# Kernel optimization log

Measured on AMD Instinct MI355X. Metric: run time of the kernel, lower is better.

The kernel has to match this reference:

```python
import jax, jax.numpy as jnp
import numpy as np

CAP_FACTOR = 1.25


def _moe_top1(x, wg, w1, b1, w2, b2):
    """Top-1 switch MoE with capacity-based token dropping.
    x: [T, d]; wg: [d, E]; w1: [E, d, f]; b1: [E, f]; w2: [E, f, d]; b2: [E, d].
    """
    T, d = x.shape
    E = wg.shape[1]
    cap = int(CAP_FACTOR * T / E)
    probs = jax.nn.softmax(x @ wg, axis=-1)            # [T, E]
    idx = jnp.argmax(probs, axis=-1)                   # [T] expert assignment
    gate = jnp.max(probs, axis=-1)                     # [T] gate prob
    oh = jax.nn.one_hot(idx, E, dtype=jnp.int32)       # [T, E]
    # position of each token within its expert's buffer
    pos = (jnp.cumsum(oh, axis=0) * oh).sum(-1) - 1    # [T]
    keep = pos < cap                                   # drop tokens over capacity
    pos_w = jnp.where(keep, pos, cap)                  # dropped -> overflow slot
    # dispatch: scatter tokens into per-expert buffers [E, cap+1, d]
    buf = jnp.zeros((E, cap + 1, d), dtype=x.dtype).at[idx, pos_w].set(x)
    buf = buf[:, :cap]                                 # slice off overflow slot
    # grouped expert FFN
    h = jax.nn.relu(jnp.einsum('ecd,edf->ecf', buf, w1) + b1[:, None, :])
    eo = jnp.einsum('ecf,efd->ecd', h, w2) + b2[:, None, :]
    # combine: gather each token's expert output, scale by gate prob, zero dropped
    pos_g = jnp.minimum(pos_w, cap - 1)
    out = eo[idx, pos_g] * (gate * keep.astype(x.dtype))[:, None]
    return out


def setup_inputs():
    key = jax.random.key(0)
    ks = jax.random.split(key, 12)
    B, S, d, dff, E1, E2 = 8, 2048, 1024, 4096, 8, 16
    s = lambda fan: np.float32(1.0 / np.sqrt(fan))
    return dict(
        x=jax.random.normal(ks[0], (B, S, d), jnp.float32),
        y=jax.random.randint(ks[1], (B,), 0, d),
        wg1=jax.random.normal(ks[2], (d, E1), jnp.float32) * s(d),
        w1a=jax.random.normal(ks[3], (E1, d, dff), jnp.float32) * s(d),
        b1a=jnp.zeros((E1, dff), jnp.float32),
        w2a=jax.random.normal(ks[4], (E1, dff, d), jnp.float32) * s(dff),
        b2a=jnp.zeros((E1, d), jnp.float32),
        wg2=jax.random.normal(ks[5], (d, E2), jnp.float32) * s(d),
        w1b=jax.random.normal(ks[6], (E2, d, dff), jnp.float32) * s(d),
        b1b=jnp.zeros((E2, dff), jnp.float32),
        w2b=jax.random.normal(ks[7], (E2, dff, d), jnp.float32) * s(dff),
        b2b=jnp.zeros((E2, d), jnp.float32),
    )


def reference(x, y, wg1, w1a, b1a, w2a, b2a, wg2, w1b, b1b, w2b, b2b):
    B, S, d = x.shape
    xf = x.reshape(B * S, d)
    m1 = _moe_top1(xf, wg1, w1a, b1a, w2a, b2a)        # moe1(x)
    m2 = _moe_top1(m1, wg2, w1b, b1b, w2b, b2b)        # moe2(moe_out)
    resid = x + m2.reshape(B, S, d)                    # residual add
    sent = resid.mean(axis=1)                          # [B, d] mean-pool -> logits
    logp = jax.nn.log_softmax(sent, axis=-1)
    return -logp[jnp.arange(B), y].mean()              # cross-entropy loss
```

## Files before the change

kernel.cpp:

```cpp
#include <hip/hip_runtime.h>
#include <hip/hip_bf16.h>
#include <cstdint>
#include <cstddef>

#define B_    8
#define S_    2048
#define D_    1024
#define DFF_  4096
#define E1_   8
#define E2_   16
#define T_    (B_*S_)
#define CAP1_ 2560
#define CAP2_ 1280
#define EC_   20480

typedef __bf16 bf16x8 __attribute__((ext_vector_type(8)));
typedef float  f32x4  __attribute__((ext_vector_type(4)));

__device__ __forceinline__ unsigned short f2bf(float x) {
  return __builtin_bit_cast(unsigned short, (__bf16)x);
}

template<int E>
__global__ __launch_bounds__(256)
void gate_kernel(const float* __restrict__ X, const float* __restrict__ WG,
                 int* __restrict__ idxO, float* __restrict__ gateO) {
  const int lane = threadIdx.x & 63;
  const int wv   = threadIdx.x >> 6;
  const int t    = blockIdx.x * 4 + wv;
  const float* xr = X + (size_t)t * D_;
  float acc[E];
#pragma unroll
  for (int e = 0; e < E; ++e) acc[e] = 0.f;
#pragma unroll
  for (int i = 0; i < 4; ++i) {
    float4 xv = *(const float4*)(xr + i * 256 + lane * 4);
    int kb = i * 256 + lane * 4;
#pragma unroll
    for (int j = 0; j < 4; ++j) {
      float xs = (&xv.x)[j];
      const float* wr = WG + (size_t)(kb + j) * E;
#pragma unroll
      for (int e = 0; e < E; ++e) acc[e] += xs * wr[e];
    }
  }
#pragma unroll
  for (int e = 0; e < E; ++e) {
    float v = acc[e];
#pragma unroll
    for (int s = 32; s >= 1; s >>= 1) v += __shfl_xor(v, s, 64);
    acc[e] = v;
  }
  if (lane == 0) {
    float mx = acc[0]; int mi = 0;
#pragma unroll
    for (int e = 1; e < E; ++e) if (acc[e] > mx) { mx = acc[e]; mi = e; }
    float s = 0.f;
#pragma unroll
    for (int e = 0; e < E; ++e) s += expf(acc[e] - mx);
    idxO[t]  = mi;
    gateO[t] = 1.0f / s;
  }
}

__global__ __launch_bounds__(1024)
void scan_kernel(const int* __restrict__ idx, int E, int cap,
                 int* __restrict__ pos, int* __restrict__ kept) {
  __shared__ int cnt[16][17];
  __shared__ int gbase[16];
  const int tid = threadIdx.x;
  const int w = tid >> 6, lane = tid & 63;
  if (tid < E) gbase[tid] = 0;
  __syncthreads();
  const unsigned long long lt = (lane == 63) ? 0xFFFFFFFFFFFFFFFFull >> 1
                                             : ((1ull << lane) - 1ull);
  for (int it = 0; it < T_ / 1024; ++it) {
    int t = it * 1024 + tid;
    int mi = idx[t];
    int rank = 0;
    for (int e = 0; e < E; ++e) {
      unsigned long long m = __ballot(mi == e);
      if (lane == 0) cnt[w][e] = __popcll(m);
      if (mi == e) rank = __popcll(m & lt);
    }
    __syncthreads();
    int off = 0;
    for (int w2 = 0; w2 < w; ++w2) off += cnt[w2][mi];
    pos[t] = gbase[mi] + off + rank;
    __syncthreads();
    if (tid < E) {
      int tot = 0;
      for (int w2 = 0; w2 < 16; ++w2) tot += cnt[w2][tid];
      gbase[tid] += tot;
    }
    __syncthreads();
  }
  if (tid < E) kept[tid] = min(gbase[tid], cap);
}

__global__ __launch_bounds__(64)
void scatter_kernel(const float* __restrict__ X, const int* __restrict__ idx,
                    const int* __restrict__ pos, int cap,
                    unsigned short* __restrict__ xbuf, int* __restrict__ tokmap,
                    float* __restrict__ mzero) {
  const int t = blockIdx.x;
  const int lane = threadIdx.x;
  const int p = pos[t];
  if (p < cap) {
    const size_t dst = ((size_t)idx[t] * cap + p) * D_;
    const float* xr = X + (size_t)t * D_;
#pragma unroll
    for (int i = 0; i < 4; ++i) {
      float4 v = *(const float4*)(xr + i * 256 + lane * 4);
      ushort4 o;
      o.x = f2bf(v.x); o.y = f2bf(v.y); o.z = f2bf(v.z); o.w = f2bf(v.w);
      *(ushort4*)(xbuf + dst + i * 256 + lane * 4) = o;
    }
    if (lane == 0) tokmap[(size_t)idx[t] * cap + p] = t;
  } else {
    float4 z = {0.f, 0.f, 0.f, 0.f};
    float* mr = mzero + (size_t)t * D_;
#pragma unroll
    for (int i = 0; i < 4; ++i) *(float4*)(mr + i * 256 + lane * 4) = z;
  }
}

__global__ __launch_bounds__(256)
void wtrans_kernel(const float* __restrict__ src, unsigned short* __restrict__ dst,
                   int K, int N) {
  __shared__ float t[64][65];
  const int tid = threadIdx.x;
  const size_t eo = (size_t)blockIdx.z * K * N;
  const int k0 = blockIdx.y * 64, n0 = blockIdx.x * 64;
  const float* s = src + eo + (size_t)k0 * N + n0;
  unsigned short* d = dst + eo + (size_t)n0 * K + k0;
#pragma unroll
  for (int i = 0; i < 4; ++i) {
    int k = i * 16 + (tid >> 4);
    int n4 = (tid & 15) * 4;
    float4 v = *(const float4*)(s + (size_t)k * N + n4);
    t[k][n4] = v.x; t[k][n4 + 1] = v.y; t[k][n4 + 2] = v.z; t[k][n4 + 3] = v.w;
  }
  __syncthreads();
#pragma unroll
  for (int i = 0; i < 4; ++i) {
    int n = i * 16 + (tid >> 4);
    int k4 = (tid & 15) * 4;
    ushort4 o;
    o.x = f2bf(t[k4][n]);     o.y = f2bf(t[k4 + 1][n]);
    o.z = f2bf(t[k4 + 2][n]); o.w = f2bf(t[k4 + 3][n]);
    *(ushort4*)(d + (size_t)n * K + k4) = o;
  }
}

template<int MODE>
__global__ __launch_bounds__(256)
void moe_gemm(const unsigned short* __restrict__ A,
              const unsigned short* __restrict__ BT,
              const float* __restrict__ bias, int K, int N, int cap, int nbcnt,
              const int* __restrict__ kept,
              unsigned short* __restrict__ Hout, float* __restrict__ Mout,
              const int* __restrict__ tokmap, const float* __restrict__ gate) {
  __shared__ char smem[16384];
  char* As = smem;
  char* Bs = smem + 8192;
  const int tid  = threadIdx.x;
  const int lane = tid & 63;
  const int wv   = tid >> 6;
  const int wr   = wv >> 1, wc = wv & 1;

  const int nwg = gridDim.x;
  const int wg  = (blockIdx.x & 7) * (nwg >> 3) + (blockIdx.x >> 3);
  const int per_grp = nbcnt * 4;
  const int grp = wg / per_grp;
  const int rem = wg - grp * per_grp;
  const int mb  = grp * 4 + (rem & 3);
  const int nb  = rem >> 2;

  const int e  = (mb * 128) / cap;
  const int r0 = mb * 128 - e * cap;
  const int kept_e = kept[e];
  if (r0 >= kept_e) return;
  const unsigned short* Ab = A + (size_t)(mb * 128) * K;
  const unsigned short* Bb = BT + ((size_t)e * N + (size_t)nb * 128) * K;

  f32x4 acc[4][4];
#pragma unroll
  for (int m = 0; m < 4; ++m)
#pragma unroll
    for (int n = 0; n < 4; ++n) acc[m][n] = (f32x4){0.f, 0.f, 0.f, 0.f};

  const int srow = tid >> 2;
  const int scb  = (tid & 3) * 16;

  for (int k0 = 0; k0 < K; k0 += 32) {
#pragma unroll
    for (int p = 0; p < 2; ++p) {
      const int row = p * 64 + srow;
      const int sw  = scb ^ ((row & 3) << 4);
      const unsigned short* ga = Ab + (size_t)row * K + k0 + (sw >> 1);
      const unsigned short* gb = Bb + (size_t)row * K + k0 + (sw >> 1);
      char* la = As + (size_t)(p * 256 + (tid & ~63)) * 16;
      char* lb = Bs + (size_t)(p * 256 + (tid & ~63)) * 16;
      __builtin_amdgcn_global_load_lds((const __attribute__((address_space(1))) void*)ga,
                                       (__attribute__((address_space(3))) void*)la,
                                       16, 0, 0);
      __builtin_amdgcn_global_load_lds((const __attribute__((address_space(1))) void*)gb,
                                       (__attribute__((address_space(3))) void*)lb,
                                       16, 0, 0);
    }
    __syncthreads();

    bf16x8 af[4], bfr[4];
    const int g16 = (lane >> 4) * 16;
    const int r16 = lane & 15;
#pragma unroll
    for (int m = 0; m < 4; ++m) {
      const int row = wr * 64 + m * 16 + r16;
      af[m] = *(const bf16x8*)(As + row * 64 + (g16 ^ ((row & 3) << 4)));
      const int col = wc * 64 + m * 16 + r16;
      bfr[m] = *(const bf16x8*)(Bs + col * 64 + (g16 ^ ((col & 3) << 4)));
    }
#pragma unroll
    for (int m = 0; m < 4; ++m)
#pragma unroll
      for (int n = 0; n < 4; ++n)
        acc[m][n] = __builtin_amdgcn_mfma_f32_16x16x32_bf16(af[m], bfr[n], acc[m][n], 0, 0, 0);
    __syncthreads();
  }

  const int r16 = lane & 15, rg = lane >> 4;
  float bv[4];
#pragma unroll
  for (int n = 0; n < 4; ++n)
    bv[n] = bias[(size_t)e * N + nb * 128 + wc * 64 + n * 16 + r16];

#pragma unroll
  for (int m = 0; m < 4; ++m) {
#pragma unroll
    for (int r = 0; r < 4; ++r) {
      const int lrow = wr * 64 + m * 16 + rg * 4 + r;
      if (MODE == 0) {
        unsigned short* orow = Hout + (size_t)(mb * 128 + lrow) * N + nb * 128;
#pragma unroll
        for (int n = 0; n < 4; ++n) {
          float v = acc[m][n][r] + bv[n];
          orow[wc * 64 + n * 16 + r16] = f2bf(fmaxf(v, 0.f));
        }
      } else {
        const int lr = r0 + lrow;
        if (lr < kept_e) {
          const int tok = tokmap[mb * 128 + lrow];
          const float gsc = gate[tok];
          float* orow = Mout + (size_t)tok * N + nb * 128;
#pragma unroll
          for (int n = 0; n < 4; ++n)
            orow[wc * 64 + n * 16 + r16] = (acc[m][n][r] + bv[n]) * gsc;
        }
      }
    }
  }
}

__global__ __launch_bounds__(256)
void reduce_kernel(const float* __restrict__ X, const float* __restrict__ M2,
                   float* __restrict__ sent) {
  const int c = blockIdx.x * 256 + threadIdx.x;
  const int b = blockIdx.z;
  const int s0 = blockIdx.y * 128;
  float a = 0.f;
  size_t base = ((size_t)b * S_ + s0) * D_ + c;
  for (int s = 0; s < 128; ++s) a += X[base + (size_t)s * D_] + M2[base + (size_t)s * D_];
  atomicAdd(&sent[b * D_ + c], a * (1.0f / (float)S_));
}

__global__ __launch_bounds__(64)
void loss_kernel(const float* __restrict__ sent, const int* __restrict__ y,
                 float* __restrict__ out) {
  const int lane = threadIdx.x;
  float total = 0.f;
  for (int b = 0; b < B_; ++b) {
    const float* s = sent + b * D_;
    float v[16];
    float mx = -1e30f;
#pragma unroll
    for (int i = 0; i < 16; ++i) { v[i] = s[lane + i * 64]; mx = fmaxf(mx, v[i]); }
#pragma unroll
    for (int sh = 32; sh >= 1; sh >>= 1) mx = fmaxf(mx, __shfl_xor(mx, sh, 64));
    float sm = 0.f;
#pragma unroll
    for (int i = 0; i < 16; ++i) sm += expf(v[i] - mx);
#pragma unroll
    for (int sh = 32; sh >= 1; sh >>= 1) sm += __shfl_xor(sm, sh, 64);
    total += logf(sm) + mx - s[y[b]];
  }
  if (lane == 0) out[0] = total * (1.0f / (float)B_);
}

extern "C" void kernel_launch(void* const* d_in, const int* in_sizes, int n_in,
                              void* d_out, int out_size, void* d_ws, size_t ws_size,
                              hipStream_t stream) {
  const float* x   = (const float*)d_in[0];
  const int*   y   = (const int*)d_in[1];
  const float* wg1 = (const float*)d_in[2];
  const float* w1a = (const float*)d_in[3];
  const float* b1a = (const float*)d_in[4];
  const float* w2a = (const float*)d_in[5];
  const float* b2a = (const float*)d_in[6];
  const float* wg2 = (const float*)d_in[7];
  const float* w1b = (const float*)d_in[8];
  const float* b1b = (const float*)d_in[9];
  const float* w2b = (const float*)d_in[10];
  const float* b2b = (const float*)d_in[11];
  float* out = (float*)d_out;
  (void)in_sizes; (void)n_in; (void)out_size; (void)ws_size;

  char* base = (char*)d_ws;
  size_t o = 0;
  auto alloc = [&](size_t bytes) { size_t r = o; o = (o + bytes + 255) & ~(size_t)255; return r; };
  int*   idx1    = (int*)  (base + alloc((size_t)T_ * 4));
  int*   pos1    = (int*)  (base + alloc((size_t)T_ * 4));
  float* gate1   = (float*)(base + alloc((size_t)T_ * 4));
  int*   idx2    = (int*)  (base + alloc((size_t)T_ * 4));
  int*   pos2    = (int*)  (base + alloc((size_t)T_ * 4));
  float* gate2   = (float*)(base + alloc((size_t)T_ * 4));
  int*   kept1   = (int*)  (base + alloc(64 * 4));
  int*   kept2   = (int*)  (base + alloc(64 * 4));
  int*   tokmap1 = (int*)  (base + alloc((size_t)EC_ * 4));
  int*   tokmap2 = (int*)  (base + alloc((size_t)EC_ * 4));
  float* sent    = (float*)(base + alloc((size_t)B_ * D_ * 4));
  float* m1      = (float*)(base + alloc((size_t)T_ * D_ * 4));
  unsigned short* xbuf = (unsigned short*)(base + alloc((size_t)EC_ * D_ * 2));
  unsigned short* h    = (unsigned short*)(base + alloc((size_t)EC_ * DFF_ * 2));
  unsigned short* wT   = (unsigned short*)(base + alloc((size_t)E2_ * D_ * DFF_ * 2));

  hipMemsetAsync(sent, 0, (size_t)B_ * D_ * 4, stream);

  gate_kernel<E1_><<<T_ / 4, 256, 0, stream>>>(x, wg1, idx1, gate1);
  scan_kernel<<<1, 1024, 0, stream>>>(idx1, E1_, CAP1_, pos1, kept1);
  scatter_kernel<<<T_, 64, 0, stream>>>(x, idx1, pos1, CAP1_, xbuf, tokmap1, m1);
  wtrans_kernel<<<dim3(DFF_ / 64, D_ / 64, E1_), 256, 0, stream>>>(w1a, wT, D_, DFF_);
  moe_gemm<0><<<(DFF_ / 128) * (EC_ / 128), 256, 0, stream>>>(
      xbuf, wT, b1a, D_, DFF_, CAP1_, DFF_ / 128, kept1, h, nullptr, nullptr, nullptr);
  wtrans_kernel<<<dim3(D_ / 64, DFF_ / 64, E1_), 256, 0, stream>>>(w2a, wT, DFF_, D_);
  moe_gemm<1><<<(D_ / 128) * (EC_ / 128), 256, 0, stream>>>(
      h, wT, b2a, DFF_, D_, CAP1_, D_ / 128, kept1, nullptr, m1, tokmap1, gate1);

  gate_kernel<E2_><<<T_ / 4, 256, 0, stream>>>(m1, wg2, idx2, gate2);
  scan_kernel<<<1, 1024, 0, stream>>>(idx2, E2_, CAP2_, pos2, kept2);
  scatter_kernel<<<T_, 64, 0, stream>>>(m1, idx2, pos2, CAP2_, xbuf, tokmap2, m1);
  wtrans_kernel<<<dim3(DFF_ / 64, D_ / 64, E2_), 256, 0, stream>>>(w1b, wT, D_, DFF_);
  moe_gemm<0><<<(DFF_ / 128) * (EC_ / 128), 256, 0, stream>>>(
      xbuf, wT, b1b, D_, DFF_, CAP2_, DFF_ / 128, kept2, h, nullptr, nullptr, nullptr);
  wtrans_kernel<<<dim3(D_ / 64, DFF_ / 64, E2_), 256, 0, stream>>>(w2b, wT, DFF_, D_);
  moe_gemm<1><<<(D_ / 128) * (EC_ / 128), 256, 0, stream>>>(
      h, wT, b2b, DFF_, D_, CAP2_, D_ / 128, kept2, nullptr, m1, tokmap2, gate2);

  reduce_kernel<<<dim3(D_ / 256, S_ / 128, B_), 256, 0, stream>>>(x, m1, sent);
  loss_kernel<<<1, 64, 0, stream>>>(sent, y, out);
}
```

Measured before the change: 1.542 ms.

## Double-buffer LDS staging with BK=64 and MFMA priority in MoE GEMM

Result: faster. 1.381 ms (-10.4%).

```diff
diff --git a/kernel.cpp b/kernel.cpp
--- a/kernel.cpp
+++ b/kernel.cpp
@@ -154,16 +154,14 @@
 }
 
 template<int MODE>
-__global__ __launch_bounds__(256)
+__global__ __launch_bounds__(256, 2)
 void moe_gemm(const unsigned short* __restrict__ A,
               const unsigned short* __restrict__ BT,
               const float* __restrict__ bias, int K, int N, int cap, int nbcnt,
               const int* __restrict__ kept,
               unsigned short* __restrict__ Hout, float* __restrict__ Mout,
               const int* __restrict__ tokmap, const float* __restrict__ gate) {
-  __shared__ char smem[16384];
-  char* As = smem;
-  char* Bs = smem + 8192;
+  __shared__ char smem[65536];
   const int tid  = threadIdx.x;
   const int lane = tid & 63;
   const int wv   = tid >> 6;
@@ -190,18 +188,17 @@
 #pragma unroll
     for (int n = 0; n < 4; ++n) acc[m][n] = (f32x4){0.f, 0.f, 0.f, 0.f};
 
-  const int srow = tid >> 2;
-  const int scb  = (tid & 3) * 16;
-
-  for (int k0 = 0; k0 < K; k0 += 32) {
-#pragma unroll
-    for (int p = 0; p < 2; ++p) {
-      const int row = p * 64 + srow;
-      const int sw  = scb ^ ((row & 3) << 4);
-      const unsigned short* ga = Ab + (size_t)row * K + k0 + (sw >> 1);
-      const unsigned short* gb = Bb + (size_t)row * K + k0 + (sw >> 1);
-      char* la = As + (size_t)(p * 256 + (tid & ~63)) * 16;
-      char* lb = Bs + (size_t)(p * 256 + (tid & ~63)) * 16;
+  auto stage = [&](int buf, int k0) {
+#pragma unroll
+    for (int j = 0; j < 4; ++j) {
+      const int c   = j * 256 + tid;
+      const int row = c >> 3;
+      const int cc  = c & 7;
+      const int scol = (cc ^ (row & 7)) << 3;
+      const unsigned short* ga = Ab + (size_t)row * K + k0 + scol;
+      const unsigned short* gb = Bb + (size_t)row * K + k0 + scol;
+      char* la = smem + buf * 32768 + (j * 256 + (tid & ~63)) * 16;
+      char* lb = la + 16384;
       __builtin_amdgcn_global_load_lds((const __attribute__((address_space(1))) void*)ga,
                                        (__attribute__((address_space(3))) void*)la,
                                        16, 0, 0);
@@ -209,27 +206,52 @@
                                        (__attribute__((address_space(3))) void*)lb,
                                        16, 0, 0);
     }
-    __syncthreads();
-
-    bf16x8 af[4], bfr[4];
-    const int g16 = (lane >> 4) * 16;
-    const int r16 = lane & 15;
+  };
+
+  const int NT = K >> 6;
+  stage(0, 0);
+  __syncthreads();
+  int cur = 0;
+
+  const int g16 = (lane >> 4) * 16;
+  const int r16 = lane & 15;
+
+  for (int t = 0; t < NT; ++t) {
+    if (t + 1 < NT) stage(cur ^ 1, (t + 1) << 6);
+
+    const char* As = smem + cur * 32768;
+    const char* Bs = As + 16384;
+    bf16x8 af[4][2], bfr[4][2];
 #pragma unroll
     for (int m = 0; m < 4; ++m) {
       const int row = wr * 64 + m * 16 + r16;
-      af[m] = *(const bf16x8*)(As + row * 64 + (g16 ^ ((row & 3) << 4)));
-      const int col = wc * 64 + m * 16 + r16;
-      bfr[m] = *(const bf16x8*)(Bs + col * 64 + (g16 ^ ((col & 3) << 4)));
-    }
-#pragma unroll
-    for (int m = 0; m < 4; ++m)
-#pragma unroll
-      for (int n = 0; n < 4; ++n)
-        acc[m][n] = __builtin_amdgcn_mfma_f32_16x16x32_bf16(af[m], bfr[n], acc[m][n], 0, 0, 0);
+      const int sw  = (row & 7) << 4;
+#pragma unroll
+      for (int ks = 0; ks < 2; ++ks)
+        af[m][ks] = *(const bf16x8*)(As + row * 128 + ((ks * 64 + g16) ^ sw));
+    }
+#pragma unroll
+    for (int n = 0; n < 4; ++n) {
+      const int row = wc * 64 + n * 16 + r16;
+      const int sw  = (row & 7) << 4;
+#pragma unroll
+      for (int ks = 0; ks < 2; ++ks)
+        bfr[n][ks] = *(const bf16x8*)(Bs + row * 128 + ((ks * 64 + g16) ^ sw));
+    }
+    __builtin_amdgcn_s_setprio(1);
+#pragma unroll
+    for (int ks = 0; ks < 2; ++ks)
+#pragma unroll
+      for (int m = 0; m < 4; ++m)
+#pragma unroll
+        for (int n = 0; n < 4; ++n)
+          acc[m][n] = __builtin_amdgcn_mfma_f32_16x16x32_bf16(af[m][ks], bfr[n][ks], acc[m][n], 0, 0, 0);
+    __builtin_amdgcn_s_setprio(0);
     __syncthreads();
-  }
-
-  const int r16 = lane & 15, rg = lane >> 4;
+    cur ^= 1;
+  }
+
+  const int rg = lane >> 4;
   float bv[4];
 #pragma unroll
   for (int n = 0; n < 4; ++n)
```

## Rewrite MoE GEMM with 256x256 tiles and a double-buffered LDS pipeline

Applied to the files above, without the earlier changes.

Measured after the change: 1.293 ms. -16.2%, faster.

```diff
diff --git a/kernel.cpp b/kernel.cpp
--- a/kernel.cpp
+++ b/kernel.cpp
@@ -153,21 +153,56 @@
   }
 }
 
+#define STG(BASEPTR, H, KT, SLOT) do {                                          \
+    const unsigned short* _s = (BASEPTR) + (size_t)((H) * 128) * K + (KT) + st_off; \
+    __builtin_amdgcn_global_load_lds((const __attribute__((address_space(1))) void*)_s, \
+        (__attribute__((address_space(3))) void*)(smem + (SLOT) + dst0), 16, 0, 0);   \
+    __builtin_amdgcn_global_load_lds((const __attribute__((address_space(1))) void*)(_s + (size_t)64 * K), \
+        (__attribute__((address_space(3))) void*)(smem + (SLOT) + 8192 + dst0), 16, 0, 0); \
+  } while (0)
+
+#define RDA(BUF, MH) do { _Pragma("unroll")                                     \
+    for (int m_ = 0; m_ < 4; ++m_) {                                            \
+      const char* _p = smem + (BUF) * 65536 + aslot + ((MH) * 4 + m_) * 2048;   \
+      af[m_][0] = *(const bf16x8*)(_p + va);                                    \
+      af[m_][1] = *(const bf16x8*)(_p + (va ^ 64)); } } while (0)
+
+#define RDB(BUF, NH) do { _Pragma("unroll")                                     \
+    for (int j_ = 0; j_ < 2; ++j_) {                                            \
+      const char* _p = smem + (BUF) * 65536 + bslot + ((NH) * 2 + j_) * 2048;   \
+      bf[(NH) * 2 + j_][0] = *(const bf16x8*)(_p + vb);                         \
+      bf[(NH) * 2 + j_][1] = *(const bf16x8*)(_p + (vb ^ 64)); } } while (0)
+
+#define QUAD(MH, NH) do {                                                       \
+    __builtin_amdgcn_s_setprio(1);                                              \
+    _Pragma("unroll") for (int m_ = 0; m_ < 4; ++m_)                            \
+    _Pragma("unroll") for (int j_ = 0; j_ < 2; ++j_)                            \
+    _Pragma("unroll") for (int k_ = 0; k_ < 2; ++k_)                            \
+      acc[(MH) * 4 + m_][(NH) * 2 + j_] = __builtin_amdgcn_mfma_f32_16x16x32_bf16( \
+          af[m_][k_], bf[(NH) * 2 + j_][k_], acc[(MH) * 4 + m_][(NH) * 2 + j_], 0, 0, 0); \
+    __builtin_amdgcn_s_setprio(0);                                              \
+  } while (0)
+
+#define LGKM0 do { asm volatile("s_waitcnt lgkmcnt(0)" ::: "memory");           \
+                   __builtin_amdgcn_sched_barrier(0); } while (0)
+#define BAR   __builtin_amdgcn_s_barrier()
+#define VM4   asm volatile("s_waitcnt vmcnt(4)" ::: "memory")
+#define VM0   asm volatile("s_waitcnt vmcnt(0)" ::: "memory")
+
 template<int MODE>
-__global__ __launch_bounds__(256)
+__global__ __launch_bounds__(512, 2)
 void moe_gemm(const unsigned short* __restrict__ A,
               const unsigned short* __restrict__ BT,
               const float* __restrict__ bias, int K, int N, int cap, int nbcnt,
               const int* __restrict__ kept,
               unsigned short* __restrict__ Hout, float* __restrict__ Mout,
               const int* __restrict__ tokmap, const float* __restrict__ gate) {
-  __shared__ char smem[16384];
-  char* As = smem;
-  char* Bs = smem + 8192;
+  __shared__ char smem[131072];
   const int tid  = threadIdx.x;
   const int lane = tid & 63;
   const int wv   = tid >> 6;
-  const int wr   = wv >> 1, wc = wv & 1;
+  const int wr   = wv >> 2;
+  const int wc   = wv & 3;
 
   const int nwg = gridDim.x;
   const int wg  = (blockIdx.x & 7) * (nwg >> 3) + (blockIdx.x >> 3);
@@ -177,71 +212,86 @@
   const int mb  = grp * 4 + (rem & 3);
   const int nb  = rem >> 2;
 
-  const int e  = (mb * 128) / cap;
-  const int r0 = mb * 128 - e * cap;
+  const int e  = (mb * 256) / cap;
+  const int r0 = mb * 256 - e * cap;
   const int kept_e = kept[e];
   if (r0 >= kept_e) return;
-  const unsigned short* Ab = A + (size_t)(mb * 128) * K;
-  const unsigned short* Bb = BT + ((size_t)e * N + (size_t)nb * 128) * K;
-
-  f32x4 acc[4][4];
-#pragma unroll
-  for (int m = 0; m < 4; ++m)
+  const unsigned short* Ab = A + (size_t)(mb * 256) * K;
+  const unsigned short* Bb = BT + ((size_t)e * N + (size_t)nb * 256) * K;
+
+  f32x4 acc[8][4];
+#pragma unroll
+  for (int m = 0; m < 8; ++m)
 #pragma unroll
     for (int n = 0; n < 4; ++n) acc[m][n] = (f32x4){0.f, 0.f, 0.f, 0.f};
 
-  const int srow = tid >> 2;
-  const int scb  = (tid & 3) * 16;
-
-  for (int k0 = 0; k0 < K; k0 += 32) {
-#pragma unroll
-    for (int p = 0; p < 2; ++p) {
-      const int row = p * 64 + srow;
-      const int sw  = scb ^ ((row & 3) << 4);
-      const unsigned short* ga = Ab + (size_t)row * K + k0 + (sw >> 1);
-      const unsigned short* gb = Bb + (size_t)row * K + k0 + (sw >> 1);
-      char* la = As + (size_t)(p * 256 + (tid & ~63)) * 16;
-      char* lb = Bs + (size_t)(p * 256 + (tid & ~63)) * 16;
-      __builtin_amdgcn_global_load_lds((const __attribute__((address_space(1))) void*)ga,
-                                       (__attribute__((address_space(3))) void*)la,
-                                       16, 0, 0);
-      __builtin_amdgcn_global_load_lds((const __attribute__((address_space(1))) void*)gb,
-                                       (__attribute__((address_space(3))) void*)lb,
-                                       16, 0, 0);
-    }
-    __syncthreads();
-
-    bf16x8 af[4], bfr[4];
-    const int g16 = (lane >> 4) * 16;
-    const int r16 = lane & 15;
-#pragma unroll
-    for (int m = 0; m < 4; ++m) {
-      const int row = wr * 64 + m * 16 + r16;
-      af[m] = *(const bf16x8*)(As + row * 64 + (g16 ^ ((row & 3) << 4)));
-      const int col = wc * 64 + m * 16 + r16;
-      bfr[m] = *(const bf16x8*)(Bs + col * 64 + (g16 ^ ((col & 3) << 4)));
-    }
-#pragma unroll
-    for (int m = 0; m < 4; ++m)
-#pragma unroll
-      for (int n = 0; n < 4; ++n)
-        acc[m][n] = __builtin_amdgcn_mfma_f32_16x16x32_bf16(af[m], bfr[n], acc[m][n], 0, 0, 0);
-    __syncthreads();
-  }
-
-  const int r16 = lane & 15, rg = lane >> 4;
+  const int scol   = ((tid & 7) ^ ((tid >> 3) & 7)) * 8;
+  const size_t st_off = (size_t)(tid >> 3) * K + scol;
+  const int dst0   = tid * 16;
+
+  const int r16 = lane & 15;
+  const int g16 = (lane >> 4) * 16;
+  const int swz = (r16 & 7) * 16;
+  const int va  = r16 * 128 + (g16 ^ swz);
+  const int vb  = (wc & 1) * 8192 + va;
+  const int aslot = wr * 16384;
+  const int bslot = 32768 + (wc >> 1) * 16384;
+  bf16x8 af[4][2], bf[4][2];
+
+  STG(Ab, 0, 0, 0);
+  STG(Ab, 1, 0, 16384);
+  STG(Bb, 0, 0, 32768);
+  STG(Bb, 1, 0, 49152);
+  STG(Bb, 0, 64, 65536 + 32768);
+  STG(Bb, 1, 64, 65536 + 49152);
+  VM4; BAR;
+
+  const int NI = K >> 7;
+  for (int i = 0; i < NI; ++i) {
+    const bool last = (i == NI - 1);
+    const int kt1 = (2 * i + 1) << 6;
+    const int kt2 = (2 * i + 2) << 6;
+    const int kt3 = (2 * i + 3) << 6;
+
+    RDA(0, 0); RDB(0, 0);
+    STG(Ab, 0, kt1, 65536);
+    BAR; LGKM0; QUAD(0, 0); BAR;
+    RDB(0, 1);
+    STG(Ab, 1, kt1, 65536 + 16384);
+    BAR; LGKM0; QUAD(0, 1); BAR;
+    RDA(0, 1);
+    if (!last) STG(Bb, 0, kt2, 32768);
+    BAR; LGKM0; QUAD(1, 1); BAR;
+    if (!last) { STG(Bb, 1, kt2, 49152); VM4; } else { VM0; }
+    BAR; __builtin_amdgcn_sched_barrier(0);
+    QUAD(1, 0); BAR;
+    RDA(1, 0); RDB(1, 0);
+    if (!last) STG(Ab, 0, kt2, 0);
+    BAR; LGKM0; QUAD(0, 0); BAR;
+    RDB(1, 1);
+    if (!last) STG(Ab, 1, kt2, 16384);
+    BAR; LGKM0; QUAD(0, 1); BAR;
+    RDA(1, 1);
+    if (!last) STG(Bb, 0, kt3, 65536 + 32768);
+    BAR; LGKM0; QUAD(1, 1); BAR;
+    if (!last) { STG(Bb, 1, kt3, 65536 + 49152); VM4; }
+    BAR; __builtin_amdgcn_sched_barrier(0);
+    QUAD(1, 0); BAR;
+  }
+
+  const int rg = lane >> 4;
   float bv[4];
 #pragma unroll
   for (int n = 0; n < 4; ++n)
-    bv[n] = bias[(size_t)e * N + nb * 128 + wc * 64 + n * 16 + r16];
-
-#pragma unroll
-  for (int m = 0; m < 4; ++m) {
+    bv[n] = bias[(size_t)e * N + nb * 256 + wc * 64 + n * 16 + r16];
+
+#pragma unroll
+  for (int m = 0; m < 8; ++m) {
 #pragma unroll
     for (int r = 0; r < 4; ++r) {
-      const int lrow = wr * 64 + m * 16 + rg * 4 + r;
+      const int lrow = wr * 128 + m * 16 + rg * 4 + r;
       if (MODE == 0) {
-        unsigned short* orow = Hout + (size_t)(mb * 128 + lrow) * N + nb * 128;
+        unsigned short* orow = Hout + (size_t)(mb * 256 + lrow) * N + nb * 256;
 #pragma unroll
         for (int n = 0; n < 4; ++n) {
           float v = acc[m][n][r] + bv[n];
@@ -250,9 +300,9 @@
       } else {
         const int lr = r0 + lrow;
         if (lr < kept_e) {
-          const int tok = tokmap[mb * 128 + lrow];
+          const int tok = tokmap[mb * 256 + lrow];
           const float gsc = gate[tok];
-          float* orow = Mout + (size_t)tok * N + nb * 128;
+          float* orow = Mout + (size_t)tok * N + nb * 256;
 #pragma unroll
           for (int n = 0; n < 4; ++n)
             orow[wc * 64 + n * 16 + r16] = (acc[m][n][r] + bv[n]) * gsc;
@@ -340,21 +390,21 @@
   scan_kernel<<<1, 1024, 0, stream>>>(idx1, E1_, CAP1_, pos1, kept1);
   scatter_kernel<<<T_, 64, 0, stream>>>(x, idx1, pos1, CAP1_, xbuf, tokmap1, m1);
   wtrans_kernel<<<dim3(DFF_ / 64, D_ / 64, E1_), 256, 0, stream>>>(w1a, wT, D_, DFF_);
-  moe_gemm<0><<<(DFF_ / 128) * (EC_ / 128), 256, 0, stream>>>(
-      xbuf, wT, b1a, D_, DFF_, CAP1_, DFF_ / 128, kept1, h, nullptr, nullptr, nullptr);
+  moe_gemm<0><<<(DFF_ / 256) * (EC_ / 256), 512, 0, stream>>>(
+      xbuf, wT, b1a, D_, DFF_, CAP1_, DFF_ / 256, kept1, h, nullptr, nullptr, nullptr);
   wtrans_kernel<<<dim3(D_ / 64, DFF_ / 64, E1_), 256, 0, stream>>>(w2a, wT, DFF_, D_);
-  moe_gemm<1><<<(D_ / 128) * (EC_ / 128), 256, 0, stream>>>(
-      h, wT, b2a, DFF_, D_, CAP1_, D_ / 128, kept1, nullptr, m1, tokmap1, gate1);
+  moe_gemm<1><<<(D_ / 256) * (EC_ / 256), 512, 0, stream>>>(
+      h, wT, b2a, DFF_, D_, CAP1_, D_ / 256, kept1, nullptr, m1, tokmap1, gate1);
 
   gate_kernel<E2_><<<T_ / 4, 256, 0, stream>>>(m1, wg2, idx2, gate2);
   scan_kernel<<<1, 1024, 0, stream>>>(idx2, E2_, CAP2_, pos2, kept2);
   scatter_kernel<<<T_, 64, 0, stream>>>(m1, idx2, pos2, CAP2_, xbuf, tokmap2, m1);
   wtrans_kernel<<<dim3(DFF_ / 64, D_ / 64, E2_), 256, 0, stream>>>(w1b, wT, D_, DFF_);
-  moe_gemm<0><<<(DFF_ / 128) * (EC_ / 128), 256, 0, stream>>>(
-      xbuf, wT, b1b, D_, DFF_, CAP2_, DFF_ / 128, kept2, h, nullptr, nullptr, nullptr);
+  moe_gemm<0><<<(DFF_ / 256) * (EC_ / 256), 512, 0, stream>>>(
+      xbuf, wT, b1b, D_, DFF_, CAP2_, DFF_ / 256, kept2, h, nullptr, nullptr, nullptr);
   wtrans_kernel<<<dim3(D_ / 64, DFF_ / 64, E2_), 256, 0, stream>>>(w2b, wT, DFF_, D_);
-  moe_gemm<1><<<(D_ / 128) * (EC_ / 128), 256, 0, stream>>>(
-      h, wT, b2b, DFF_, D_, CAP2_, D_ / 128, kept2, nullptr, m1, tokmap2, gate2);
+  moe_gemm<1><<<(D_ / 256) * (EC_ / 256), 512, 0, stream>>>(
+      h, wT, b2b, DFF_, D_, CAP2_, D_ / 256, kept2, nullptr, m1, tokmap2, gate2);
 
   reduce_kernel<<<dim3(D_ / 256, S_ / 128, B_), 256, 0, stream>>>(x, m1, sent);
   loss_kernel<<<1, 64, 0, stream>>>(sent, y, out);
```
